# Kernel tuning notes

Hardware: AMD Instinct MI355X
Metric: run time of the kernel (lower is better)

Reference implementation:

```python
import jax, jax.numpy as jnp
import numpy as np
from jax import lax

KERNEL_SIZE = 11
SIGMA = 1.5
K1 = 0.01
K2 = 0.03
DATA_RANGE = 1.0


def _gaussian_kernel(size, sigma):
    coords = np.arange(size, dtype=np.float32) - (size - 1) / 2.0
    g = np.exp(-(coords[None, :] ** 2 + coords[:, None] ** 2) / (2.0 * sigma ** 2))
    g = g / g.sum()
    return jnp.asarray(g, dtype=jnp.float32)  # [k, k]


def _dwconv(x, k2d):
    # depthwise valid conv, groups = C (matches F.conv2d(..., groups=C))
    C = x.shape[1]
    w = jnp.broadcast_to(k2d[None, None], (C, 1, k2d.shape[0], k2d.shape[1]))
    return lax.conv_general_dilated(
        x, w, window_strides=(1, 1), padding='VALID',
        dimension_numbers=('NCHW', 'OIHW', 'NCHW'), feature_group_count=C)


def _avg_pool(x, f):
    # torch F.avg_pool2d(x, kernel_size=f) : stride=f, floor mode
    s = lax.reduce_window(x, 0.0, lax.add, (1, 1, f, f), (1, 1, f, f), 'VALID')
    return s / float(f * f)


def setup_inputs() -> dict:
    key = jax.random.key(0)
    kx, ky = jax.random.split(key)
    x = jax.random.uniform(kx, (32, 3, 512, 512), dtype=jnp.float32)
    y = jax.random.uniform(ky, (32, 3, 512, 512), dtype=jnp.float32)
    return {"x": x, "y": y}


def reference(x, y):
    x = x / DATA_RANGE
    y = y / DATA_RANGE
    # average-pool to roughly 256 resolution before SSIM (downsample=True)
    f = max(1, int(round(min(x.shape[-2], x.shape[-1]) / 256.0)))
    if f > 1:
        x = _avg_pool(x, f)
        y = _avg_pool(y, f)
    kern = _gaussian_kernel(KERNEL_SIZE, SIGMA)
    c1 = K1 ** 2
    c2 = K2 ** 2
    mu_x = _dwconv(x, kern)
    mu_y = _dwconv(y, kern)
    mu_xx = mu_x * mu_x
    mu_yy = mu_y * mu_y
    mu_xy = mu_x * mu_y
    sigma_xx = _dwconv(x * x, kern) - mu_xx
    sigma_yy = _dwconv(y * y, kern) - mu_yy
    sigma_xy = _dwconv(x * y, kern) - mu_xy
    cs = (2.0 * sigma_xy + c2) / (sigma_xx + sigma_yy + c2)
    ss = (2.0 * mu_xy + c1) / (mu_xx + mu_yy + c1) * cs
    ssim_val = ss.mean(axis=(-1, -2))          # [B, C]
    ssim_val = ssim_val.mean(axis=1)           # [B] mean over channels
    score = ssim_val.mean(axis=0)              # reduction='mean' over batch
    return 1.0 - score
```

## Files before the change

### kernel.cpp

```cpp
#include <hip/hip_runtime.h>


#define KS 11
#define H 12
#define ROWS (H + KS - 1)
#define NSTRIP 21
#define NPLANE 96
#define NWAVE (NPLANE * NSTRIP)
#define NBLOCK (NWAVE / 4)
#define OUTD 246
#define BUFW 272
#define C1V 1e-4f
#define C2V 9e-4f

__device__ __forceinline__ void load_pool(const float* __restrict__ xp,
                                          const float* __restrict__ yp,
                                          int r0, int i, int lane,
                                          float (&px)[4], float (&py)[4]) {
    int pr = r0 + i; pr = pr > 255 ? 255 : pr;
    const float* xr = xp + (size_t)(2 * pr) * 512 + 8 * lane;
    const float* yr = yp + (size_t)(2 * pr) * 512 + 8 * lane;
    float4 a0 = *(const float4*)xr;
    float4 a1 = *(const float4*)(xr + 4);
    float4 b0 = *(const float4*)(xr + 512);
    float4 b1 = *(const float4*)(xr + 516);
    float4 c0 = *(const float4*)yr;
    float4 c1 = *(const float4*)(yr + 4);
    float4 d0 = *(const float4*)(yr + 512);
    float4 d1 = *(const float4*)(yr + 516);
    px[0] = (a0.x + a0.y + b0.x + b0.y) * 0.25f;
    px[1] = (a0.z + a0.w + b0.z + b0.w) * 0.25f;
    px[2] = (a1.x + a1.y + b1.x + b1.y) * 0.25f;
    px[3] = (a1.z + a1.w + b1.z + b1.w) * 0.25f;
    py[0] = (c0.x + c0.y + d0.x + d0.y) * 0.25f;
    py[1] = (c0.z + c0.w + d0.z + d0.w) * 0.25f;
    py[2] = (c1.x + c1.y + d1.x + d1.y) * 0.25f;
    py[3] = (c1.z + c1.w + d1.z + d1.w) * 0.25f;
}

__device__ __forceinline__ void step_row(float* vb, const float (&wt)[KS],
                                         float (&rx)[KS][4], float (&ry)[KS][4],
                                         const float (&px)[4], const float (&py)[4],
                                         int lane, int ro, float& local) {
    #pragma unroll
    for (int c = 0; c < 4; ++c) { rx[KS - 1][c] = px[c]; ry[KS - 1][c] = py[c]; }

    float vmx[4] = {0,0,0,0}, vmy[4] = {0,0,0,0};
    float vxx[4] = {0,0,0,0}, vyy[4] = {0,0,0,0}, vxy[4] = {0,0,0,0};
    #pragma unroll
    for (int k = 0; k < KS; ++k) {
        float wk = wt[k];
        #pragma unroll
        for (int c = 0; c < 4; ++c) {
            float xv = rx[k][c], yv = ry[k][c];
            vmx[c] += wk * xv;       vmy[c] += wk * yv;
            vxx[c] += wk * xv * xv;  vyy[c] += wk * yv * yv;
            vxy[c] += wk * xv * yv;
        }
    }

    *(float4*)(vb + 0 * BUFW + 4 * lane) = make_float4(vmx[0], vmx[1], vmx[2], vmx[3]);
    *(float4*)(vb + 1 * BUFW + 4 * lane) = make_float4(vmy[0], vmy[1], vmy[2], vmy[3]);
    *(float4*)(vb + 2 * BUFW + 4 * lane) = make_float4(vxx[0], vxx[1], vxx[2], vxx[3]);
    *(float4*)(vb + 3 * BUFW + 4 * lane) = make_float4(vyy[0], vyy[1], vyy[2], vyy[3]);
    *(float4*)(vb + 4 * BUFW + 4 * lane) = make_float4(vxy[0], vxy[1], vxy[2], vxy[3]);
    __builtin_amdgcn_wave_barrier();

    float hp[5][4];
    #pragma unroll
    for (int p = 0; p < 5; ++p) {
        const float* bp = vb + p * BUFW + 4 * lane;
        float4 q0 = *(const float4*)bp;
        float4 q1 = *(const float4*)(bp + 4);
        float4 q2 = *(const float4*)(bp + 8);
        float4 q3 = *(const float4*)(bp + 12);
        float win[16] = {q0.x, q0.y, q0.z, q0.w, q1.x, q1.y, q1.z, q1.w,
                         q2.x, q2.y, q2.z, q2.w, q3.x, q3.y, q3.z, q3.w};
        #pragma unroll
        for (int c = 0; c < 4; ++c) {
            float a = 0.f;
            #pragma unroll
            for (int j = 0; j < KS; ++j) a += wt[j] * win[c + j];
            hp[p][c] = a;
        }
    }

    if (ro < OUTD) {
        #pragma unroll
        for (int c = 0; c < 4; ++c) {
            int oc = 4 * lane + c;
            float mx = hp[0][c], my = hp[1][c];
            float mxx = mx * mx, myy = my * my, mxy = mx * my;
            float sxx = hp[2][c] - mxx, syy = hp[3][c] - myy, sxy = hp[4][c] - mxy;
            float num = (2.f * mxy + C1V) * (2.f * sxy + C2V);
            float den = (mxx + myy + C1V) * (sxx + syy + C2V);
            float ss = num / den;
            local += (oc < OUTD) ? ss : 0.f;
        }
    }

    #pragma unroll
    for (int k = 0; k < KS - 1; ++k) {
        #pragma unroll
        for (int c = 0; c < 4; ++c) { rx[k][c] = rx[k + 1][c]; ry[k][c] = ry[k + 1][c]; }
    }
}

__global__ __launch_bounds__(256, 2) void ssim_wave(const float* __restrict__ x,
                                                    const float* __restrict__ y,
                                                    double* __restrict__ partial) {
    __shared__ float vbuf[4][2][5][BUFW];
    const int tid = threadIdx.x;
    const int wv = tid >> 6, lane = tid & 63;
    const int gid = blockIdx.x * 4 + wv;
    const int plane = gid / NSTRIP, strip = gid % NSTRIP;
    const int r0 = strip * H;
    const float* xp = x + (size_t)plane * (512 * 512);
    const float* yp = y + (size_t)plane * (512 * 512);

    float wt[KS];
    {
        float s = 0.f;
        #pragma unroll
        for (int i = 0; i < KS; ++i) {
            float d = (float)i - 5.f;
            wt[i] = expf(-d * d / 4.5f);
            s += wt[i];
        }
        float inv = 1.f / s;
        #pragma unroll
        for (int i = 0; i < KS; ++i) wt[i] *= inv;
    }

    if (lane < BUFW - 256) {
        #pragma unroll
        for (int b = 0; b < 2; ++b)
            #pragma unroll
            for (int p = 0; p < 5; ++p)
                vbuf[wv][b][p][256 + lane] = 0.f;
    }
    __builtin_amdgcn_wave_barrier();

    float rx[KS][4], ry[KS][4];
    #pragma unroll
    for (int i = 0; i < KS - 1; ++i)
        load_pool(xp, yp, r0, i, lane, rx[i], ry[i]);

    float cpx[4], cpy[4], npx[4], npy[4];
    load_pool(xp, yp, r0, KS - 1, lane, cpx, cpy);
    float local = 0.f;

    #pragma unroll 1
    for (int i = KS - 1; i < ROWS; ++i) {
        load_pool(xp, yp, r0, i + 1, lane, npx, npy);
        float* vb = &vbuf[wv][i & 1][0][0];
        step_row(vb, wt, rx, ry, cpx, cpy, lane, r0 + i - (KS - 1), local);
        #pragma unroll
        for (int c = 0; c < 4; ++c) { cpx[c] = npx[c]; cpy[c] = npy[c]; }
    }

    #pragma unroll
    for (int off = 32; off > 0; off >>= 1)
        local += __shfl_down(local, off, 64);
    if (lane == 0) partial[gid] = (double)local;
}

__global__ __launch_bounds__(256) void ssim_finalize(const double* __restrict__ partial,
                                                     float* __restrict__ out) {
    const int tid = threadIdx.x;
    double s = 0.0;
    for (int i = tid; i < NWAVE; i += 256) s += partial[i];
    #pragma unroll
    for (int off = 32; off > 0; off >>= 1)
        s += __shfl_down(s, off, 64);
    __shared__ double sd[4];
    if ((tid & 63) == 0) sd[tid >> 6] = s;
    __syncthreads();
    if (tid == 0) {
        double total = sd[0] + sd[1] + sd[2] + sd[3];
        const double n = (double)NPLANE * OUTD * OUTD;
        out[0] = (float)(1.0 - total / n);
    }
}

extern "C" void kernel_launch(void* const* d_in, const int* in_sizes, int n_in,
                              void* d_out, int out_size, void* d_ws, size_t ws_size,
                              hipStream_t stream) {
    const float* x = (const float*)d_in[0];
    const float* y = (const float*)d_in[1];
    float* out = (float*)d_out;
    double* partial = (double*)d_ws;

    ssim_wave<<<NBLOCK, 256, 0, stream>>>(x, y, partial);
    ssim_finalize<<<1, 256, 0, stream>>>(partial, out);
}
```

Before: 65.57 us.

## Fully unroll row loop with ring-buffer registers, shorter strips, single LDS buffer

Strip height drops from 12 to 8 rows, so there are more waves (31 strips per plane). The row loop is fully unrolled and the sliding window becomes a compile-time ring buffer, which removes the per-row register shifting. The LDS buffer is no longer double-buffered, and each lane takes its own first four vertical sums from registers instead of reloading them from LDS. The min-waves launch-bound hint is dropped. In exchange, the shorter strips add halo overhead: each strip now processes 18 input rows to produce 8 outputs, where before it was 22 for 12. This means more redundant global loads and vertical-sum work per output.

Result: slower. 93.60 us (+42.7%).

```diff
diff --git a/kernel.cpp b/kernel.cpp
--- a/kernel.cpp
+++ b/kernel.cpp
@@ -2,9 +2,9 @@
 
 
 #define KS 11
-#define H 12
+#define H 8
 #define ROWS (H + KS - 1)
-#define NSTRIP 21
+#define NSTRIP 31
 #define NPLANE 96
 #define NWAVE (NPLANE * NSTRIP)
 #define NBLOCK (NWAVE / 4)
@@ -38,78 +38,10 @@
     py[3] = (c1.z + c1.w + d1.z + d1.w) * 0.25f;
 }
 
-__device__ __forceinline__ void step_row(float* vb, const float (&wt)[KS],
-                                         float (&rx)[KS][4], float (&ry)[KS][4],
-                                         const float (&px)[4], const float (&py)[4],
-                                         int lane, int ro, float& local) {
-    #pragma unroll
-    for (int c = 0; c < 4; ++c) { rx[KS - 1][c] = px[c]; ry[KS - 1][c] = py[c]; }
-
-    float vmx[4] = {0,0,0,0}, vmy[4] = {0,0,0,0};
-    float vxx[4] = {0,0,0,0}, vyy[4] = {0,0,0,0}, vxy[4] = {0,0,0,0};
-    #pragma unroll
-    for (int k = 0; k < KS; ++k) {
-        float wk = wt[k];
-        #pragma unroll
-        for (int c = 0; c < 4; ++c) {
-            float xv = rx[k][c], yv = ry[k][c];
-            vmx[c] += wk * xv;       vmy[c] += wk * yv;
-            vxx[c] += wk * xv * xv;  vyy[c] += wk * yv * yv;
-            vxy[c] += wk * xv * yv;
-        }
-    }
-
-    *(float4*)(vb + 0 * BUFW + 4 * lane) = make_float4(vmx[0], vmx[1], vmx[2], vmx[3]);
-    *(float4*)(vb + 1 * BUFW + 4 * lane) = make_float4(vmy[0], vmy[1], vmy[2], vmy[3]);
-    *(float4*)(vb + 2 * BUFW + 4 * lane) = make_float4(vxx[0], vxx[1], vxx[2], vxx[3]);
-    *(float4*)(vb + 3 * BUFW + 4 * lane) = make_float4(vyy[0], vyy[1], vyy[2], vyy[3]);
-    *(float4*)(vb + 4 * BUFW + 4 * lane) = make_float4(vxy[0], vxy[1], vxy[2], vxy[3]);
-    __builtin_amdgcn_wave_barrier();
-
-    float hp[5][4];
-    #pragma unroll
-    for (int p = 0; p < 5; ++p) {
-        const float* bp = vb + p * BUFW + 4 * lane;
-        float4 q0 = *(const float4*)bp;
-        float4 q1 = *(const float4*)(bp + 4);
-        float4 q2 = *(const float4*)(bp + 8);
-        float4 q3 = *(const float4*)(bp + 12);
-        float win[16] = {q0.x, q0.y, q0.z, q0.w, q1.x, q1.y, q1.z, q1.w,
-                         q2.x, q2.y, q2.z, q2.w, q3.x, q3.y, q3.z, q3.w};
-        #pragma unroll
-        for (int c = 0; c < 4; ++c) {
-            float a = 0.f;
-            #pragma unroll
-            for (int j = 0; j < KS; ++j) a += wt[j] * win[c + j];
-            hp[p][c] = a;
-        }
-    }
-
-    if (ro < OUTD) {
-        #pragma unroll
-        for (int c = 0; c < 4; ++c) {
-            int oc = 4 * lane + c;
-            float mx = hp[0][c], my = hp[1][c];
-            float mxx = mx * mx, myy = my * my, mxy = mx * my;
-            float sxx = hp[2][c] - mxx, syy = hp[3][c] - myy, sxy = hp[4][c] - mxy;
-            float num = (2.f * mxy + C1V) * (2.f * sxy + C2V);
-            float den = (mxx + myy + C1V) * (sxx + syy + C2V);
-            float ss = num / den;
-            local += (oc < OUTD) ? ss : 0.f;
-        }
-    }
-
-    #pragma unroll
-    for (int k = 0; k < KS - 1; ++k) {
-        #pragma unroll
-        for (int c = 0; c < 4; ++c) { rx[k][c] = rx[k + 1][c]; ry[k][c] = ry[k + 1][c]; }
-    }
-}
-
-__global__ __launch_bounds__(256, 2) void ssim_wave(const float* __restrict__ x,
-                                                    const float* __restrict__ y,
-                                                    double* __restrict__ partial) {
-    __shared__ float vbuf[4][2][5][BUFW];
+__global__ __launch_bounds__(256) void ssim_wave(const float* __restrict__ x,
+                                                 const float* __restrict__ y,
+                                                 double* __restrict__ partial) {
+    __shared__ float vbuf[4][5][BUFW];
     const int tid = threadIdx.x;
     const int wv = tid >> 6, lane = tid & 63;
     const int gid = blockIdx.x * 4 + wv;
@@ -134,10 +66,8 @@
 
     if (lane < BUFW - 256) {
         #pragma unroll
-        for (int b = 0; b < 2; ++b)
-            #pragma unroll
-            for (int p = 0; p < 5; ++p)
-                vbuf[wv][b][p][256 + lane] = 0.f;
+        for (int p = 0; p < 5; ++p)
+            vbuf[wv][p][256 + lane] = 0.f;
     }
     __builtin_amdgcn_wave_barrier();
 
@@ -146,15 +76,89 @@
     for (int i = 0; i < KS - 1; ++i)
         load_pool(xp, yp, r0, i, lane, rx[i], ry[i]);
 
-    float cpx[4], cpy[4], npx[4], npy[4];
+    float cpx[4], cpy[4];
     load_pool(xp, yp, r0, KS - 1, lane, cpx, cpy);
+
     float local = 0.f;
-
-    #pragma unroll 1
+    float* vb = &vbuf[wv][0][0];
+
+    #pragma unroll
     for (int i = KS - 1; i < ROWS; ++i) {
-        load_pool(xp, yp, r0, i + 1, lane, npx, npy);
-        float* vb = &vbuf[wv][i & 1][0][0];
-        step_row(vb, wt, rx, ry, cpx, cpy, lane, r0 + i - (KS - 1), local);
+        float npx[4], npy[4];
+        if (i + 1 < ROWS)
+            load_pool(xp, yp, r0, i + 1, lane, npx, npy);
+
+        {
+            const int s = i % KS;
+            #pragma unroll
+            for (int c = 0; c < 4; ++c) { rx[s][c] = cpx[c]; ry[s][c] = cpy[c]; }
+        }
+
+        float vmx[4] = {0,0,0,0}, vmy[4] = {0,0,0,0};
+        float vxx[4] = {0,0,0,0}, vyy[4] = {0,0,0,0}, vxy[4] = {0,0,0,0};
+        #pragma unroll
+        for (int k = 0; k < KS; ++k) {
+            const int s = (i - (KS - 1) + k) % KS;
+            float wk = wt[k];
+            #pragma unroll
+            for (int c = 0; c < 4; ++c) {
+                float xv = rx[s][c], yv = ry[s][c];
+                vmx[c] += wk * xv;       vmy[c] += wk * yv;
+                vxx[c] += wk * xv * xv;  vyy[c] += wk * yv * yv;
+                vxy[c] += wk * xv * yv;
+            }
+        }
+
+        *(float4*)(vb + 0 * BUFW + 4 * lane) = make_float4(vmx[0], vmx[1], vmx[2], vmx[3]);
+        *(float4*)(vb + 1 * BUFW + 4 * lane) = make_float4(vmy[0], vmy[1], vmy[2], vmy[3]);
+        *(float4*)(vb + 2 * BUFW + 4 * lane) = make_float4(vxx[0], vxx[1], vxx[2], vxx[3]);
+        *(float4*)(vb + 3 * BUFW + 4 * lane) = make_float4(vyy[0], vyy[1], vyy[2], vyy[3]);
+        *(float4*)(vb + 4 * BUFW + 4 * lane) = make_float4(vxy[0], vxy[1], vxy[2], vxy[3]);
+        __builtin_amdgcn_wave_barrier();
+
+        float hp[5][4];
+        #pragma unroll
+        for (int p = 0; p < 5; ++p) {
+            const float* bp = vb + p * BUFW + 4 * lane;
+            float4 q1 = *(const float4*)(bp + 4);
+            float4 q2 = *(const float4*)(bp + 8);
+            float4 q3 = *(const float4*)(bp + 12);
+            float own0, own1, own2, own3;
+            switch (p) {
+                case 0: own0 = vmx[0]; own1 = vmx[1]; own2 = vmx[2]; own3 = vmx[3]; break;
+                case 1: own0 = vmy[0]; own1 = vmy[1]; own2 = vmy[2]; own3 = vmy[3]; break;
+                case 2: own0 = vxx[0]; own1 = vxx[1]; own2 = vxx[2]; own3 = vxx[3]; break;
+                case 3: own0 = vyy[0]; own1 = vyy[1]; own2 = vyy[2]; own3 = vyy[3]; break;
+                default: own0 = vxy[0]; own1 = vxy[1]; own2 = vxy[2]; own3 = vxy[3]; break;
+            }
+            float win[16] = {own0, own1, own2, own3,
+                             q1.x, q1.y, q1.z, q1.w,
+                             q2.x, q2.y, q2.z, q2.w,
+                             q3.x, q3.y, q3.z, q3.w};
+            #pragma unroll
+            for (int c = 0; c < 4; ++c) {
+                float a = 0.f;
+                #pragma unroll
+                for (int j = 0; j < KS; ++j) a += wt[j] * win[c + j];
+                hp[p][c] = a;
+            }
+        }
+
+        const int ro = r0 + i - (KS - 1);
+        if (ro < OUTD) {
+            #pragma unroll
+            for (int c = 0; c < 4; ++c) {
+                int oc = 4 * lane + c;
+                float mx = hp[0][c], my = hp[1][c];
+                float mxx = mx * mx, myy = my * my, mxy = mx * my;
+                float sxx = hp[2][c] - mxx, syy = hp[3][c] - myy, sxy = hp[4][c] - mxy;
+                float num = (2.f * mxy + C1V) * (2.f * sxy + C2V);
+                float den = (mxx + myy + C1V) * (sxx + syy + C2V);
+                float ss = num / den;
+                local += (oc < OUTD) ? ss : 0.f;
+            }
+        }
+
         #pragma unroll
         for (int c = 0; c < 4; ++c) { cpx[c] = npx[c]; cpy[c] = npy[c]; }
     }
```

## Split each strip across two waves with shared LDS row buffer

Applied to the files above, without the earlier changes.

Each strip, previously handled by a single wave holding four columns per lane, is now handled by a 128-thread block of two waves, each lane owning two pooled columns. The vertical pass results go into a shared LDS buffer and are synchronised with __syncthreads before the horizontal pass. The prefetch now keeps the raw float4 loads and pools them at the start of the next iteration. This doubles the wave count and halves per-thread registers to raise occupancy and latency hiding, at the cost of a block-wide barrier per row and extra overlapping LDS reads.

New measurement: 74.44 us. 1.14x slower.

```diff
diff --git a/kernel.cpp b/kernel.cpp
--- a/kernel.cpp
+++ b/kernel.cpp
@@ -6,117 +6,25 @@
 #define ROWS (H + KS - 1)
 #define NSTRIP 21
 #define NPLANE 96
-#define NWAVE (NPLANE * NSTRIP)
-#define NBLOCK (NWAVE / 4)
+#define NBLK (NPLANE * NSTRIP)
+#define NWAVE (NBLK * 2)
 #define OUTD 246
 #define BUFW 272
 #define C1V 1e-4f
 #define C2V 9e-4f
 
-__device__ __forceinline__ void load_pool(const float* __restrict__ xp,
-                                          const float* __restrict__ yp,
-                                          int r0, int i, int lane,
-                                          float (&px)[4], float (&py)[4]) {
-    int pr = r0 + i; pr = pr > 255 ? 255 : pr;
-    const float* xr = xp + (size_t)(2 * pr) * 512 + 8 * lane;
-    const float* yr = yp + (size_t)(2 * pr) * 512 + 8 * lane;
-    float4 a0 = *(const float4*)xr;
-    float4 a1 = *(const float4*)(xr + 4);
-    float4 b0 = *(const float4*)(xr + 512);
-    float4 b1 = *(const float4*)(xr + 516);
-    float4 c0 = *(const float4*)yr;
-    float4 c1 = *(const float4*)(yr + 4);
-    float4 d0 = *(const float4*)(yr + 512);
-    float4 d1 = *(const float4*)(yr + 516);
-    px[0] = (a0.x + a0.y + b0.x + b0.y) * 0.25f;
-    px[1] = (a0.z + a0.w + b0.z + b0.w) * 0.25f;
-    px[2] = (a1.x + a1.y + b1.x + b1.y) * 0.25f;
-    px[3] = (a1.z + a1.w + b1.z + b1.w) * 0.25f;
-    py[0] = (c0.x + c0.y + d0.x + d0.y) * 0.25f;
-    py[1] = (c0.z + c0.w + d0.z + d0.w) * 0.25f;
-    py[2] = (c1.x + c1.y + d1.x + d1.y) * 0.25f;
-    py[3] = (c1.z + c1.w + d1.z + d1.w) * 0.25f;
-}
-
-__device__ __forceinline__ void step_row(float* vb, const float (&wt)[KS],
-                                         float (&rx)[KS][4], float (&ry)[KS][4],
-                                         const float (&px)[4], const float (&py)[4],
-                                         int lane, int ro, float& local) {
-    #pragma unroll
-    for (int c = 0; c < 4; ++c) { rx[KS - 1][c] = px[c]; ry[KS - 1][c] = py[c]; }
-
-    float vmx[4] = {0,0,0,0}, vmy[4] = {0,0,0,0};
-    float vxx[4] = {0,0,0,0}, vyy[4] = {0,0,0,0}, vxy[4] = {0,0,0,0};
-    #pragma unroll
-    for (int k = 0; k < KS; ++k) {
-        float wk = wt[k];
-        #pragma unroll
-        for (int c = 0; c < 4; ++c) {
-            float xv = rx[k][c], yv = ry[k][c];
-            vmx[c] += wk * xv;       vmy[c] += wk * yv;
-            vxx[c] += wk * xv * xv;  vyy[c] += wk * yv * yv;
-            vxy[c] += wk * xv * yv;
-        }
-    }
-
-    *(float4*)(vb + 0 * BUFW + 4 * lane) = make_float4(vmx[0], vmx[1], vmx[2], vmx[3]);
-    *(float4*)(vb + 1 * BUFW + 4 * lane) = make_float4(vmy[0], vmy[1], vmy[2], vmy[3]);
-    *(float4*)(vb + 2 * BUFW + 4 * lane) = make_float4(vxx[0], vxx[1], vxx[2], vxx[3]);
-    *(float4*)(vb + 3 * BUFW + 4 * lane) = make_float4(vyy[0], vyy[1], vyy[2], vyy[3]);
-    *(float4*)(vb + 4 * BUFW + 4 * lane) = make_float4(vxy[0], vxy[1], vxy[2], vxy[3]);
-    __builtin_amdgcn_wave_barrier();
-
-    float hp[5][4];
-    #pragma unroll
-    for (int p = 0; p < 5; ++p) {
-        const float* bp = vb + p * BUFW + 4 * lane;
-        float4 q0 = *(const float4*)bp;
-        float4 q1 = *(const float4*)(bp + 4);
-        float4 q2 = *(const float4*)(bp + 8);
-        float4 q3 = *(const float4*)(bp + 12);
-        float win[16] = {q0.x, q0.y, q0.z, q0.w, q1.x, q1.y, q1.z, q1.w,
-                         q2.x, q2.y, q2.z, q2.w, q3.x, q3.y, q3.z, q3.w};
-        #pragma unroll
-        for (int c = 0; c < 4; ++c) {
-            float a = 0.f;
-            #pragma unroll
-            for (int j = 0; j < KS; ++j) a += wt[j] * win[c + j];
-            hp[p][c] = a;
-        }
-    }
-
-    if (ro < OUTD) {
-        #pragma unroll
-        for (int c = 0; c < 4; ++c) {
-            int oc = 4 * lane + c;
-            float mx = hp[0][c], my = hp[1][c];
-            float mxx = mx * mx, myy = my * my, mxy = mx * my;
-            float sxx = hp[2][c] - mxx, syy = hp[3][c] - myy, sxy = hp[4][c] - mxy;
-            float num = (2.f * mxy + C1V) * (2.f * sxy + C2V);
-            float den = (mxx + myy + C1V) * (sxx + syy + C2V);
-            float ss = num / den;
-            local += (oc < OUTD) ? ss : 0.f;
-        }
-    }
-
-    #pragma unroll
-    for (int k = 0; k < KS - 1; ++k) {
-        #pragma unroll
-        for (int c = 0; c < 4; ++c) { rx[k][c] = rx[k + 1][c]; ry[k][c] = ry[k + 1][c]; }
-    }
-}
-
-__global__ __launch_bounds__(256, 2) void ssim_wave(const float* __restrict__ x,
-                                                    const float* __restrict__ y,
-                                                    double* __restrict__ partial) {
-    __shared__ float vbuf[4][2][5][BUFW];
+__global__ __launch_bounds__(128) void ssim_strip(const float* __restrict__ x,
+                                                  const float* __restrict__ y,
+                                                  double* __restrict__ partial) {
+    __shared__ float vbuf[2][5][BUFW];
     const int tid = threadIdx.x;
     const int wv = tid >> 6, lane = tid & 63;
-    const int gid = blockIdx.x * 4 + wv;
+    const int gid = blockIdx.x;
     const int plane = gid / NSTRIP, strip = gid % NSTRIP;
     const int r0 = strip * H;
-    const float* xp = x + (size_t)plane * (512 * 512);
-    const float* yp = y + (size_t)plane * (512 * 512);
+    const int colbase = wv * 128 + 2 * lane;
+    const float* xp = x + (size_t)plane * 262144 + 2 * colbase;
+    const float* yp = y + (size_t)plane * 262144 + 2 * colbase;
 
     float wt[KS];
     {
@@ -132,37 +40,117 @@
         for (int i = 0; i < KS; ++i) wt[i] *= inv;
     }
 
-    if (lane < BUFW - 256) {
-        #pragma unroll
-        for (int b = 0; b < 2; ++b)
-            #pragma unroll
-            for (int p = 0; p < 5; ++p)
-                vbuf[wv][b][p][256 + lane] = 0.f;
+    for (int idx = tid; idx < 2 * 5 * 16; idx += 128) {
+        int b = idx / 80, rest = idx % 80, p = rest / 16, c = rest % 16;
+        vbuf[b][p][256 + c] = 0.f;
     }
-    __builtin_amdgcn_wave_barrier();
+    __syncthreads();
 
-    float rx[KS][4], ry[KS][4];
+    float rx[KS][2], ry[KS][2];
     #pragma unroll
-    for (int i = 0; i < KS - 1; ++i)
-        load_pool(xp, yp, r0, i, lane, rx[i], ry[i]);
+    for (int i = 0; i < KS - 1; ++i) {
+        int pr = r0 + i; pr = pr > 255 ? 255 : pr;
+        const float* xr = xp + (size_t)(2 * pr) * 512;
+        const float* yr = yp + (size_t)(2 * pr) * 512;
+        float4 a0 = *(const float4*)xr, a1 = *(const float4*)(xr + 512);
+        float4 b0 = *(const float4*)yr, b1 = *(const float4*)(yr + 512);
+        rx[i][0] = (a0.x + a0.y + a1.x + a1.y) * 0.25f;
+        rx[i][1] = (a0.z + a0.w + a1.z + a1.w) * 0.25f;
+        ry[i][0] = (b0.x + b0.y + b1.x + b1.y) * 0.25f;
+        ry[i][1] = (b0.z + b0.w + b1.z + b1.w) * 0.25f;
+    }
 
-    float cpx[4], cpy[4], npx[4], npy[4];
-    load_pool(xp, yp, r0, KS - 1, lane, cpx, cpy);
+    float4 gx0, gx1, gy0, gy1;
+    {
+        int pr = r0 + KS - 1; pr = pr > 255 ? 255 : pr;
+        const float* xr = xp + (size_t)(2 * pr) * 512;
+        const float* yr = yp + (size_t)(2 * pr) * 512;
+        gx0 = *(const float4*)xr; gx1 = *(const float4*)(xr + 512);
+        gy0 = *(const float4*)yr; gy1 = *(const float4*)(yr + 512);
+    }
+
     float local = 0.f;
 
     #pragma unroll 1
     for (int i = KS - 1; i < ROWS; ++i) {
-        load_pool(xp, yp, r0, i + 1, lane, npx, npy);
-        float* vb = &vbuf[wv][i & 1][0][0];
-        step_row(vb, wt, rx, ry, cpx, cpy, lane, r0 + i - (KS - 1), local);
+        rx[KS - 1][0] = (gx0.x + gx0.y + gx1.x + gx1.y) * 0.25f;
+        rx[KS - 1][1] = (gx0.z + gx0.w + gx1.z + gx1.w) * 0.25f;
+        ry[KS - 1][0] = (gy0.x + gy0.y + gy1.x + gy1.y) * 0.25f;
+        ry[KS - 1][1] = (gy0.z + gy0.w + gy1.z + gy1.w) * 0.25f;
+
+        if (i + 1 < ROWS) {
+            int pr = r0 + i + 1; pr = pr > 255 ? 255 : pr;
+            const float* xr = xp + (size_t)(2 * pr) * 512;
+            const float* yr = yp + (size_t)(2 * pr) * 512;
+            gx0 = *(const float4*)xr; gx1 = *(const float4*)(xr + 512);
+            gy0 = *(const float4*)yr; gy1 = *(const float4*)(yr + 512);
+        }
+
+        float vm[5][2] = {{0,0},{0,0},{0,0},{0,0},{0,0}};
         #pragma unroll
-        for (int c = 0; c < 4; ++c) { cpx[c] = npx[c]; cpy[c] = npy[c]; }
+        for (int k = 0; k < KS; ++k) {
+            float wk = wt[k];
+            #pragma unroll
+            for (int c = 0; c < 2; ++c) {
+                float xv = rx[k][c], yv = ry[k][c];
+                vm[0][c] += wk * xv;       vm[1][c] += wk * yv;
+                vm[2][c] += wk * xv * xv;  vm[3][c] += wk * yv * yv;
+                vm[4][c] += wk * xv * yv;
+            }
+        }
+
+        #pragma unroll
+        for (int k = 0; k < KS - 1; ++k) {
+            #pragma unroll
+            for (int c = 0; c < 2; ++c) { rx[k][c] = rx[k + 1][c]; ry[k][c] = ry[k + 1][c]; }
+        }
+
+        const int par = i & 1;
+        #pragma unroll
+        for (int p = 0; p < 5; ++p)
+            *(float2*)&vbuf[par][p][colbase] = make_float2(vm[p][0], vm[p][1]);
+
+        __syncthreads();
+
+        const int ro = r0 + i - (KS - 1);
+        float hp[5][2];
+        #pragma unroll
+        for (int p = 0; p < 5; ++p) {
+            const float* bp = &vbuf[par][p][colbase];
+            float w[14];
+            #pragma unroll
+            for (int j = 0; j < 7; ++j) {
+                float2 t = *(const float2*)(bp + 2 * j);
+                w[2 * j] = t.x; w[2 * j + 1] = t.y;
+            }
+            #pragma unroll
+            for (int c = 0; c < 2; ++c) {
+                float a = 0.f;
+                #pragma unroll
+                for (int j = 0; j < KS; ++j) a += wt[j] * w[c + j];
+                hp[p][c] = a;
+            }
+        }
+
+        if (ro < OUTD) {
+            #pragma unroll
+            for (int c = 0; c < 2; ++c) {
+                int oc = colbase + c;
+                float mx = hp[0][c], my = hp[1][c];
+                float mxx = mx * mx, myy = my * my, mxy = mx * my;
+                float sxx = hp[2][c] - mxx, syy = hp[3][c] - myy, sxy = hp[4][c] - mxy;
+                float num = (2.f * mxy + C1V) * (2.f * sxy + C2V);
+                float den = (mxx + myy + C1V) * (sxx + syy + C2V);
+                float ss = num / den;
+                local += (oc < OUTD) ? ss : 0.f;
+            }
+        }
     }
 
     #pragma unroll
     for (int off = 32; off > 0; off >>= 1)
         local += __shfl_down(local, off, 64);
-    if (lane == 0) partial[gid] = (double)local;
+    if (lane == 0) partial[gid * 2 + wv] = (double)local;
 }
 
 __global__ __launch_bounds__(256) void ssim_finalize(const double* __restrict__ partial,
@@ -191,6 +179,6 @@
     float* out = (float*)d_out;
     double* partial = (double*)d_ws;
 
-    ssim_wave<<<NBLOCK, 256, 0, stream>>>(x, y, partial);
+    ssim_strip<<<NBLK, 128, 0, stream>>>(x, y, partial);
     ssim_finalize<<<1, 256, 0, stream>>>(partial, out);
 }
```
